# Kernel tuning notes

Hardware: AMD Instinct MI355X
Metric: run time of the kernel (lower is better)

The kernel has to match this reference:

```python
import jax, jax.numpy as jnp
import numpy as np

K, T, D, S, A, C, H = 128, 64, 128, 512, 4, 16, 512
N_LEAVES = 128
TEMP = 1.0          # sample_merge_temp
EPS_SQRT = 1e-4     # distances.EPSILON ** 0.5 with EPSILON = 1e-8
_SQ_EPS = 1e-12     # numerical guard inside sqrt (diagonal of pairwise dists is 0)


def setup_inputs() -> dict:
    key = jax.random.key(0)
    ks = jax.random.split(key, 11)
    leaf_counts_Kxt = jax.random.randint(ks[0], (K, T), 1, 5)
    embeddings_KxtxD = jax.random.normal(ks[1], (K, T, D), jnp.float32)
    log_felsensteins_KxtxSxA = jax.random.normal(ks[2], (K, T, S, A), jnp.float32)
    site_positions_SxC = jax.random.uniform(ks[3], (S, C), jnp.float32)
    W1 = jax.random.normal(ks[4], (2 * D, H), jnp.float32) / jnp.sqrt(2.0 * D)
    b1 = jnp.zeros((H,), jnp.float32)
    W2 = jax.random.normal(ks[5], (H, D), jnp.float32) / jnp.sqrt(1.0 * H)
    b2 = jnp.zeros((D,), jnp.float32)
    gumbel_Kxtt = jax.random.gumbel(ks[6], (K, T * T), jnp.float32)
    u1_K = jax.random.uniform(ks[7], (K,), jnp.float32, minval=1e-6, maxval=1.0)
    u2_K = jax.random.uniform(ks[8], (K,), jnp.float32, minval=1e-6, maxval=1.0)
    return {
        "N": N_LEAVES,
        "leaf_counts_Kxt": leaf_counts_Kxt,
        "embeddings_KxtxD": embeddings_KxtxD,
        "log_felsensteins_KxtxSxA": log_felsensteins_KxtxSxA,
        "site_positions_SxC": site_positions_SxC,
        "W1": W1, "b1": b1, "W2": W2, "b2": b2,
        "gumbel_Kxtt": gumbel_Kxtt, "u1_K": u1_K, "u2_K": u2_K,
    }


def _merge_encoder(c1_KxD, c2_KxD, W1, b1, W2, b2):
    # MLP merge encoder: MLP(concat(child1, child2)) -> parent embedding
    h = jax.nn.relu(jnp.concatenate([c1_KxD, c2_KxD], axis=-1) @ W1 + b1)
    return h @ W2 + b2


def reference(N, leaf_counts_Kxt, embeddings_KxtxD, log_felsensteins_KxtxSxA,
              site_positions_SxC, W1, b1, W2, b2, gumbel_Kxtt, u1_K, u2_K):
    Kp, t = leaf_counts_Kxt.shape
    ar = jnp.arange(Kp)

    # --- pairwise distances over all t*t subtree pairs per particle ---
    diff_Kxtxtxd = embeddings_KxtxD[:, :, None, :] - embeddings_KxtxD[:, None, :, :]
    pd_Kxtxt = jnp.sqrt(jnp.sum(diff_Kxtxtxd * diff_Kxtxtxd, axis=-1) + _SQ_EPS)
    merge_log_weights_Kxtxt = -pd_Kxtxt / TEMP
    # diagonal_scatter(-inf): forbid self-merges
    eye = jnp.eye(t, dtype=bool)[None]
    merge_log_weights_Kxtxt = jnp.where(eye, -jnp.inf, merge_log_weights_Kxtxt)

    # --- categorical merge sampling (gumbel-max with pre-drawn noise) ---
    flat_Kxtt = merge_log_weights_Kxtxt.reshape(Kp, t * t)
    sample_K = jnp.argmax(flat_Kxtt + gumbel_Kxtt, axis=1)
    idx1_K = sample_K // t
    idx2_K = sample_K % t
    log_merge_prob_K = (flat_Kxtt[ar, sample_K] + jnp.log(2.0)
                        - jax.scipy.special.logsumexp(flat_Kxtt, axis=1))

    # --- merged embedding ---
    child1_KxD = embeddings_KxtxD[ar, idx1_K]
    child2_KxD = embeddings_KxtxD[ar, idx2_K]
    embedding_KxD = _merge_encoder(child1_KxD, child2_KxD, W1, b1, W2, b2)

    # --- branch lengths sampled from Exp(rate = 1/(dist + eps)) ---
    d1_K = jnp.sqrt(jnp.sum((child1_KxD - embedding_KxD) ** 2, axis=-1) + _SQ_EPS)
    d2_K = jnp.sqrt(jnp.sum((child2_KxD - embedding_KxD) ** 2, axis=-1) + _SQ_EPS)
    rate1_K = 1.0 / (d1_K + EPS_SQRT)
    rate2_K = 1.0 / (d2_K + EPS_SQRT)
    branch1_K = -(1.0 / rate1_K) * jnp.log(u1_K)
    branch2_K = -(1.0 / rate2_K) * jnp.log(u2_K)
    log_branch1_prior_K = jnp.log(rate1_K) - rate1_K * branch1_K
    log_branch2_prior_K = jnp.log(rate2_K) - rate2_K * branch2_K

    log_v_plus_K = log_merge_prob_K + log_branch1_prior_K + log_branch2_prior_K

    # --- over-counting correction ---
    ones_K = jnp.sum(leaf_counts_Kxt == 1, axis=1)
    ones_K = ones_K - (leaf_counts_Kxt[ar, idx1_K] == 1).astype(ones_K.dtype)
    ones_K = ones_K - (leaf_counts_Kxt[ar, idx2_K] == 1).astype(ones_K.dtype)
    log_v_minus_K = jnp.log((N - ones_K).astype(jnp.float32))

    return (idx1_K, idx2_K, branch1_K, branch2_K, embedding_KxD,
            log_v_plus_K, log_v_minus_K)
```

## Files before the change

kernel.cpp:

```cpp
#include <hip/hip_runtime.h>
#include <math.h>

#define Kp 128
#define Tn 64
#define Dn 128
#define Hn 512
#define RS 136

typedef __attribute__((ext_vector_type(8))) short short8;
typedef __attribute__((ext_vector_type(4))) float f32x4;

__global__ __launch_bounds__(512, 1) void ep_kernel(
    const int*   __restrict__ Nptr,
    const int*   __restrict__ leaf,
    const float* __restrict__ emb,
    const float* __restrict__ W1,
    const float* __restrict__ b1,
    const float* __restrict__ W2,
    const float* __restrict__ b2,
    const float* __restrict__ gum,
    const float* __restrict__ u1,
    const float* __restrict__ u2,
    float* __restrict__ out)
{
    const int k    = blockIdx.x;
    const int tid  = threadIdx.x;
    const int lane = tid & 63;
    const int wid  = tid >> 6;

    __shared__ unsigned short EH[Tn * RS];
    __shared__ unsigned short EL[Tn * RS];
    __shared__ float xs[256];
    __shared__ float hsh[Hn];
    __shared__ float buf[2112];
    __shared__ float nI[Tn];
    __shared__ float sBest[8]; __shared__ int sIdx[8]; __shared__ float sW[8];
    __shared__ float sSum[8];
    __shared__ float sD1[2]; __shared__ float sD2[2];
    __shared__ int   sOnes;
    __shared__ int   fIdx; __shared__ float fW;
    __shared__ float embs[Dn];

    const bool gw   = (wid < 4);
    const int itp   = (wid >> 1) & 1;
    const int jtp   = wid & 1;
    const int lrow  = lane & 15;
    const int lq    = lane >> 4;

    if (tid < 64) {
        unsigned long long m = __ballot(leaf[k * Tn + tid] == 1);
        if (tid == 0) sOnes = __popcll(m);
    }

    float4 ev[4];
    {
        const float4* src = (const float4*)(emb + (size_t)k * Tn * Dn);
        #pragma unroll
        for (int it = 0; it < 4; ++it) ev[it] = src[tid + it * 512];
    }
    float gv[16];
    if (gw) {
        const float* gk = gum + (size_t)k * (Tn * Tn);
        #pragma unroll
        for (int a = 0; a < 2; ++a)
            #pragma unroll
            for (int b = 0; b < 2; ++b) {
                int it = 2 * itp + a, jt = 2 * jtp + b;
                int col = jt * 16 + lrow;
                #pragma unroll
                for (int r = 0; r < 4; ++r) {
                    int row = it * 16 + lq * 4 + r;
                    gv[(a * 2 + b) * 4 + r] = gk[row * Tn + col];
                }
            }
    }

    #pragma unroll
    for (int it = 0; it < 4; ++it) {
        int f4 = tid + it * 512;
        int i  = f4 >> 5;
        int d0 = (f4 & 31) << 2;
        float4 v = ev[it];
        unsigned short hx = __float_as_uint(v.x) >> 16, hy = __float_as_uint(v.y) >> 16,
                       hz = __float_as_uint(v.z) >> 16, hw = __float_as_uint(v.w) >> 16;
        float rx = v.x - __uint_as_float((unsigned int)hx << 16);
        float ry = v.y - __uint_as_float((unsigned int)hy << 16);
        float rz = v.z - __uint_as_float((unsigned int)hz << 16);
        float rw = v.w - __uint_as_float((unsigned int)hw << 16);
        unsigned short lx = __float_as_uint(rx) >> 16, ly = __float_as_uint(ry) >> 16,
                       lz = __float_as_uint(rz) >> 16, lw = __float_as_uint(rw) >> 16;
        *(ushort4*)&EH[i * RS + d0] = make_ushort4(hx, hy, hz, hw);
        *(ushort4*)&EL[i * RS + d0] = make_ushort4(lx, ly, lz, lw);
    }
    __syncthreads();

    f32x4 acc[2][2] = {};
    if (gw) {
        const int ka = lq * 8;
        #pragma unroll
        for (int ks = 0; ks < 4; ++ks) {
            int kb  = ks * 32 + ka;
            int ra0 = ((2 * itp + 0) * 16 + lrow) * RS + kb;
            int ra1 = ra0 + 16 * RS;
            int rb0 = ((2 * jtp + 0) * 16 + lrow) * RS + kb;
            int rb1 = rb0 + 16 * RS;
            short8 ah0 = *(const short8*)&EH[ra0], ah1 = *(const short8*)&EH[ra1];
            short8 al0 = *(const short8*)&EL[ra0], al1 = *(const short8*)&EL[ra1];
            short8 bh0 = *(const short8*)&EH[rb0], bh1 = *(const short8*)&EH[rb1];
            short8 bl0 = *(const short8*)&EL[rb0], bl1 = *(const short8*)&EL[rb1];
            acc[0][0] = __builtin_amdgcn_mfma_f32_16x16x32_bf16(ah0, bh0, acc[0][0], 0, 0, 0);
            acc[0][1] = __builtin_amdgcn_mfma_f32_16x16x32_bf16(ah0, bh1, acc[0][1], 0, 0, 0);
            acc[1][0] = __builtin_amdgcn_mfma_f32_16x16x32_bf16(ah1, bh0, acc[1][0], 0, 0, 0);
            acc[1][1] = __builtin_amdgcn_mfma_f32_16x16x32_bf16(ah1, bh1, acc[1][1], 0, 0, 0);
            acc[0][0] = __builtin_amdgcn_mfma_f32_16x16x32_bf16(ah0, bl0, acc[0][0], 0, 0, 0);
            acc[0][1] = __builtin_amdgcn_mfma_f32_16x16x32_bf16(ah0, bl1, acc[0][1], 0, 0, 0);
            acc[1][0] = __builtin_amdgcn_mfma_f32_16x16x32_bf16(ah1, bl0, acc[1][0], 0, 0, 0);
            acc[1][1] = __builtin_amdgcn_mfma_f32_16x16x32_bf16(ah1, bl1, acc[1][1], 0, 0, 0);
            acc[0][0] = __builtin_amdgcn_mfma_f32_16x16x32_bf16(al0, bh0, acc[0][0], 0, 0, 0);
            acc[0][1] = __builtin_amdgcn_mfma_f32_16x16x32_bf16(al0, bh1, acc[0][1], 0, 0, 0);
            acc[1][0] = __builtin_amdgcn_mfma_f32_16x16x32_bf16(al1, bh0, acc[1][0], 0, 0, 0);
            acc[1][1] = __builtin_amdgcn_mfma_f32_16x16x32_bf16(al1, bh1, acc[1][1], 0, 0, 0);
        }

        if (itp == jtp) {
            #pragma unroll
            for (int a = 0; a < 2; ++a) {
                if ((lrow >> 2) == lq) {
                    int c = lrow;
                    int t = 2 * itp + a;
                    f32x4 v = acc[a][a];
                    int   s = c & 3;
                    float val = (s == 0) ? v.x : (s == 1) ? v.y : (s == 2) ? v.z : v.w;
                    nI[t * 16 + c] = val;
                }
            }
        }
    }
    __syncthreads();

    float es = 0.0f, best = -INFINITY, bestW = 0.0f;
    int   bestIdx = 0;
    if (gw) {
        #pragma unroll
        for (int a = 0; a < 2; ++a)
            #pragma unroll
            for (int b = 0; b < 2; ++b) {
                int it = 2 * itp + a, jt = 2 * jtp + b;
                int col = jt * 16 + lrow;
                float njc = nI[col];
                f32x4 v = acc[a][b];
                float gvals[4] = {v.x, v.y, v.z, v.w};
                #pragma unroll
                for (int r = 0; r < 4; ++r) {
                    int row = it * 16 + lq * 4 + r;
                    float pd2 = nI[row] + njc - 2.0f * gvals[r];
                    pd2 = fmaxf(pd2, 0.0f) + 1e-12f;
                    float wv = (row == col) ? -INFINITY : -sqrtf(pd2);
                    es += expf(wv);
                    float wg = wv + gv[(a * 2 + b) * 4 + r];
                    int idx = row * Tn + col;
                    if (wg > best || (wg == best && idx < bestIdx)) {
                        best = wg; bestIdx = idx; bestW = wv;
                    }
                }
            }
    }

    #pragma unroll
    for (int off = 32; off > 0; off >>= 1) {
        float ob = __shfl_down(best, off);
        int   oi = __shfl_down(bestIdx, off);
        float ow = __shfl_down(bestW, off);
        float oe = __shfl_down(es, off);
        if (ob > best || (ob == best && oi < bestIdx)) { best = ob; bestIdx = oi; bestW = ow; }
        es += oe;
    }
    if (lane == 0) { sBest[wid] = best; sIdx[wid] = bestIdx; sW[wid] = bestW; sSum[wid] = es; }
    __syncthreads();
    if (tid == 0) {
        best = sBest[0]; bestIdx = sIdx[0]; bestW = sW[0];
        #pragma unroll
        for (int q = 1; q < 8; ++q) {
            if (sBest[q] > best || (sBest[q] == best && sIdx[q] < bestIdx)) {
                best = sBest[q]; bestIdx = sIdx[q]; bestW = sW[q];
            }
        }
        fIdx = bestIdx; fW = bestW;
    }
    __syncthreads();

    const int i1 = fIdx >> 6;
    const int i2 = fIdx & 63;

    if (tid < 256) {
        int d  = tid & 127;
        int ii = (tid < 128) ? i1 : i2;
        float hi = __uint_as_float((unsigned int)EH[ii * RS + d] << 16);
        float lo = __uint_as_float((unsigned int)EL[ii * RS + d] << 16);
        xs[tid] = hi + lo;
    }
    __syncthreads();

    {
        const int j0 = 4 * (tid & 127);
        const int ih = tid >> 7;
        const float* W1r = W1 + j0;
        float4 a = {0, 0, 0, 0};
        const int ib = ih * 64;
        #pragma unroll 4
        for (int i = ib; i < ib + 64; i += 4) {
            float4 x  = *(const float4*)&xs[i];
            float4 w0 = *(const float4*)&W1r[(size_t)(i + 0) * Hn];
            float4 w1 = *(const float4*)&W1r[(size_t)(i + 1) * Hn];
            float4 w2 = *(const float4*)&W1r[(size_t)(i + 2) * Hn];
            float4 w3 = *(const float4*)&W1r[(size_t)(i + 3) * Hn];
            a.x += x.x * w0.x + x.y * w1.x + x.z * w2.x + x.w * w3.x;
            a.y += x.x * w0.y + x.y * w1.y + x.z * w2.y + x.w * w3.y;
            a.z += x.x * w0.z + x.y * w1.z + x.z * w2.z + x.w * w3.z;
            a.w += x.x * w0.w + x.y * w1.w + x.z * w2.w + x.w * w3.w;
        }
        *(float4*)&buf[ih * 516 + j0] = a;
    }
    __syncthreads();
    hsh[tid] = fmaxf(b1[tid] + buf[tid] + buf[516 + tid]
                     + buf[1032 + tid] + buf[1548 + tid], 0.0f);
    __syncthreads();

    {
        const int jh  = tid >> 5;
        const int dd4 = 4 * (tid & 31);
        float4 a = {0, 0, 0, 0};
        const int jb = jh * 32;
        #pragma unroll 4
        for (int j = jb; j < jb + 32; j += 4) {
            float4 h4 = *(const float4*)&hsh[j];
            float4 w0 = *(const float4*)&W2[(size_t)(j + 0) * Dn + dd4];
            float4 w1 = *(const float4*)&W2[(size_t)(j + 1) * Dn + dd4];
            float4 w2 = *(const float4*)&W2[(size_t)(j + 2) * Dn + dd4];
            float4 w3 = *(const float4*)&W2[(size_t)(j + 3) * Dn + dd4];
            a.x += h4.x * w0.x + h4.y * w1.x + h4.z * w2.x + h4.w * w3.x;
            a.y += h4.x * w0.y + h4.y * w1.y + h4.z * w2.y + h4.w * w3.y;
            a.z += h4.x * w0.z + h4.y * w1.z + h4.z * w2.z + h4.w * w3.z;
            a.w += h4.x * w0.w + h4.y * w1.w + h4.z * w2.w + h4.w * w3.w;
        }
        *(float4*)&buf[jh * 132 + dd4] = a;
    }
    __syncthreads();
    if (tid < 128) {
        float e = b2[tid];
        #pragma unroll
        for (int p = 0; p < 16; ++p) e += buf[p * 132 + tid];
        embs[tid] = e;
        out[4 * Kp + k * Dn + tid] = e;
    }
    __syncthreads();

    if (tid < 128) {
        float e  = embs[tid];
        float q1 = xs[tid] - e;        float v1 = q1 * q1;
        float q2 = xs[128 + tid] - e;  float v2 = q2 * q2;
        #pragma unroll
        for (int off = 32; off > 0; off >>= 1) {
            v1 += __shfl_down(v1, off);
            v2 += __shfl_down(v2, off);
        }
        if (lane == 0) { sD1[wid] = v1; sD2[wid] = v2; }
    }
    __syncthreads();

    if (tid == 0) {
        float s1 = sD1[0] + sD1[1];
        float s2 = sD2[0] + sD2[1];
        float d1 = sqrtf(s1 + 1e-12f);
        float d2 = sqrtf(s2 + 1e-12f);
        float rate1 = 1.0f / (d1 + 1e-4f);
        float rate2 = 1.0f / (d2 + 1e-4f);
        float branch1 = -(1.0f / rate1) * logf(u1[k]);
        float branch2 = -(1.0f / rate2) * logf(u2[k]);
        float lbp1 = logf(rate1) - rate1 * branch1;
        float lbp2 = logf(rate2) - rate2 * branch2;
        float ssum = sSum[0] + sSum[1] + sSum[2] + sSum[3]
                   + sSum[4] + sSum[5] + sSum[6] + sSum[7];
        float lse  = logf(ssum);
        float lmp  = fW + 0.69314718055994531f - lse;
        float lvp  = lmp + lbp1 + lbp2;
        int lc1 = leaf[k * Tn + i1];
        int lc2 = leaf[k * Tn + i2];
        int ones = sOnes - (lc1 == 1 ? 1 : 0) - (lc2 == 1 ? 1 : 0);
        float lvm = logf((float)(Nptr[0] - ones));

        out[k]                         = (float)i1;
        out[Kp + k]                    = (float)i2;
        out[2 * Kp + k]                = branch1;
        out[3 * Kp + k]                = branch2;
        out[4 * Kp + Kp * Dn + k]      = lvp;
        out[4 * Kp + Kp * Dn + Kp + k] = lvm;
    }
}

extern "C" void kernel_launch(void* const* d_in, const int* in_sizes, int n_in,
                              void* d_out, int out_size, void* d_ws, size_t ws_size,
                              hipStream_t stream) {
    const int*   Nptr = (const int*)  d_in[0];
    const int*   leaf = (const int*)  d_in[1];
    const float* emb  = (const float*)d_in[2];
    const float* W1   = (const float*)d_in[5];
    const float* b1   = (const float*)d_in[6];
    const float* W2   = (const float*)d_in[7];
    const float* b2   = (const float*)d_in[8];
    const float* gum  = (const float*)d_in[9];
    const float* u1   = (const float*)d_in[10];
    const float* u2   = (const float*)d_in[11];
    float* out = (float*)d_out;

    ep_kernel<<<Kp, 512, 0, stream>>>(Nptr, leaf, emb, W1, b1, W2, b2, gum, u1, u2, out);
}
```

Before: 126.5 us.

## Prefetch MLP weights early, compute norms in fp32, and drop block barriers

Row squared norms are now computed in fp32 with shuffles during staging instead of being read from the MFMA diagonal, which removes one barrier. The first chunks of W1 and W2 are loaded into registers before the distance MFMA so their global latency overlaps that compute. The final argmax reduction is done redundantly by every thread, and child embeddings are rebuilt directly from the bf16 hi/lo shared arrays, which removes the xs/embs staging and several barriers. Small scalars (biases, u1/u2, N, leaf counts) are also loaded early. In exchange, register pressure goes up, and the fp32 norms may differ slightly from the MFMA-derived ones.

```diff
diff --git a/kernel.cpp b/kernel.cpp
--- a/kernel.cpp
+++ b/kernel.cpp
@@ -9,6 +9,10 @@
 
 typedef __attribute__((ext_vector_type(8))) short short8;
 typedef __attribute__((ext_vector_type(4))) float f32x4;
+
+__device__ __forceinline__ float bfpair(unsigned int hi_bits, unsigned int lo_bits) {
+    return __uint_as_float(hi_bits) + __uint_as_float(lo_bits);
+}
 
 __global__ __launch_bounds__(512, 1) void ep_kernel(
     const int*   __restrict__ Nptr,
@@ -30,16 +34,14 @@
 
     __shared__ unsigned short EH[Tn * RS];
     __shared__ unsigned short EL[Tn * RS];
-    __shared__ float xs[256];
     __shared__ float hsh[Hn];
     __shared__ float buf[2112];
     __shared__ float nI[Tn];
     __shared__ float sBest[8]; __shared__ int sIdx[8]; __shared__ float sW[8];
     __shared__ float sSum[8];
     __shared__ float sD1[2]; __shared__ float sD2[2];
+    __shared__ int   sLeaf[Tn];
     __shared__ int   sOnes;
-    __shared__ int   fIdx; __shared__ float fW;
-    __shared__ float embs[Dn];
 
     const bool gw   = (wid < 4);
     const int itp   = (wid >> 1) & 1;
@@ -47,8 +49,18 @@
     const int lrow  = lane & 15;
     const int lq    = lane >> 4;
 
+    const int j0  = 4 * (tid & 127);
+    const int ih  = tid >> 7;
+    const int ib  = ih * 64;
+    const float* W1r = W1 + j0;
+    const int jh  = tid >> 5;
+    const int jb  = jh * 32;
+    const int dd4 = 4 * (tid & 31);
+
     if (tid < 64) {
-        unsigned long long m = __ballot(leaf[k * Tn + tid] == 1);
+        int lc = leaf[k * Tn + tid];
+        sLeaf[tid] = lc;
+        unsigned long long m = __ballot(lc == 1);
         if (tid == 0) sOnes = __popcll(m);
     }
 
@@ -74,6 +86,10 @@
                 }
             }
     }
+    float b1v = b1[tid];
+    float b2v = (tid < 128) ? b2[tid] : 0.0f;
+    float u1v = 0.0f, u2v = 0.0f; int Nv = 0;
+    if (tid == 0) { u1v = u1[k]; u2v = u2[k]; Nv = Nptr[0]; }
 
     #pragma unroll
     for (int it = 0; it < 4; ++it) {
@@ -91,8 +107,23 @@
                        lz = __float_as_uint(rz) >> 16, lw = __float_as_uint(rw) >> 16;
         *(ushort4*)&EH[i * RS + d0] = make_ushort4(hx, hy, hz, hw);
         *(ushort4*)&EL[i * RS + d0] = make_ushort4(lx, ly, lz, lw);
-    }
-    __syncthreads();
+        float s = v.x * v.x + v.y * v.y + v.z * v.z + v.w * v.w;
+        s += __shfl_down(s, 16, 32);
+        s += __shfl_down(s,  8, 32);
+        s += __shfl_down(s,  4, 32);
+        s += __shfl_down(s,  2, 32);
+        s += __shfl_down(s,  1, 32);
+        if ((lane & 31) == 0) nI[i] = s;
+    }
+    __syncthreads();
+
+    float4 w1p[16];
+    #pragma unroll
+    for (int p = 0; p < 16; ++p) w1p[p] = *(const float4*)&W1r[(size_t)(ib + p) * Hn];
+    float4 w2p[8];
+    #pragma unroll
+    for (int p = 0; p < 8; ++p)  w2p[p] = *(const float4*)&W2[(size_t)(jb + p) * Dn + dd4];
+    __builtin_amdgcn_sched_barrier(0);
 
     f32x4 acc[2][2] = {};
     if (gw) {
@@ -121,22 +152,7 @@
             acc[1][0] = __builtin_amdgcn_mfma_f32_16x16x32_bf16(al1, bh0, acc[1][0], 0, 0, 0);
             acc[1][1] = __builtin_amdgcn_mfma_f32_16x16x32_bf16(al1, bh1, acc[1][1], 0, 0, 0);
         }
-
-        if (itp == jtp) {
-            #pragma unroll
-            for (int a = 0; a < 2; ++a) {
-                if ((lrow >> 2) == lq) {
-                    int c = lrow;
-                    int t = 2 * itp + a;
-                    f32x4 v = acc[a][a];
-                    int   s = c & 3;
-                    float val = (s == 0) ? v.x : (s == 1) ? v.y : (s == 2) ? v.z : v.w;
-                    nI[t * 16 + c] = val;
-                }
-            }
-        }
-    }
-    __syncthreads();
+    }
 
     float es = 0.0f, best = -INFINITY, bestW = 0.0f;
     int   bestIdx = 0;
@@ -165,7 +181,6 @@
                 }
             }
     }
-
     #pragma unroll
     for (int off = 32; off > 0; off >>= 1) {
         float ob = __shfl_down(best, off);
@@ -177,88 +192,100 @@
     }
     if (lane == 0) { sBest[wid] = best; sIdx[wid] = bestIdx; sW[wid] = bestW; sSum[wid] = es; }
     __syncthreads();
-    if (tid == 0) {
-        best = sBest[0]; bestIdx = sIdx[0]; bestW = sW[0];
-        #pragma unroll
-        for (int q = 1; q < 8; ++q) {
-            if (sBest[q] > best || (sBest[q] == best && sIdx[q] < bestIdx)) {
-                best = sBest[q]; bestIdx = sIdx[q]; bestW = sW[q];
-            }
-        }
-        fIdx = bestIdx; fW = bestW;
-    }
-    __syncthreads();
-
-    const int i1 = fIdx >> 6;
-    const int i2 = fIdx & 63;
-
-    if (tid < 256) {
-        int d  = tid & 127;
-        int ii = (tid < 128) ? i1 : i2;
-        float hi = __uint_as_float((unsigned int)EH[ii * RS + d] << 16);
-        float lo = __uint_as_float((unsigned int)EL[ii * RS + d] << 16);
-        xs[tid] = hi + lo;
-    }
-    __syncthreads();
+
+    float gBest = sBest[0], gW = sW[0], essum = sSum[0];
+    int   gIdx = sIdx[0];
+    #pragma unroll
+    for (int q = 1; q < 8; ++q) {
+        float bq = sBest[q]; int iq = sIdx[q];
+        if (bq > gBest || (bq == gBest && iq < gIdx)) { gBest = bq; gIdx = iq; gW = sW[q]; }
+        essum += sSum[q];
+    }
+    const int i1 = gIdx >> 6;
+    const int i2 = gIdx & 63;
 
     {
-        const int j0 = 4 * (tid & 127);
-        const int ih = tid >> 7;
-        const float* W1r = W1 + j0;
+        const int ii    = (ih < 2) ? i1 : i2;
+        const int dbase = (ih & 1) * 64;
+        const unsigned short* ehr = &EH[ii * RS + dbase];
+        const unsigned short* elr = &EL[ii * RS + dbase];
         float4 a = {0, 0, 0, 0};
-        const int ib = ih * 64;
+        #pragma unroll
+        for (int r = 0; r < 16; r += 4) {
+            uint2 hu = *(const uint2*)&ehr[r];
+            uint2 lu = *(const uint2*)&elr[r];
+            float x0 = bfpair(hu.x << 16,          lu.x << 16);
+            float x1 = bfpair(hu.x & 0xFFFF0000u,  lu.x & 0xFFFF0000u);
+            float x2 = bfpair(hu.y << 16,          lu.y << 16);
+            float x3 = bfpair(hu.y & 0xFFFF0000u,  lu.y & 0xFFFF0000u);
+            float4 w0 = w1p[r + 0], w1 = w1p[r + 1], w2 = w1p[r + 2], w3 = w1p[r + 3];
+            a.x += x0 * w0.x + x1 * w1.x + x2 * w2.x + x3 * w3.x;
+            a.y += x0 * w0.y + x1 * w1.y + x2 * w2.y + x3 * w3.y;
+            a.z += x0 * w0.z + x1 * w1.z + x2 * w2.z + x3 * w3.z;
+            a.w += x0 * w0.w + x1 * w1.w + x2 * w2.w + x3 * w3.w;
+        }
         #pragma unroll 4
-        for (int i = ib; i < ib + 64; i += 4) {
-            float4 x  = *(const float4*)&xs[i];
-            float4 w0 = *(const float4*)&W1r[(size_t)(i + 0) * Hn];
-            float4 w1 = *(const float4*)&W1r[(size_t)(i + 1) * Hn];
-            float4 w2 = *(const float4*)&W1r[(size_t)(i + 2) * Hn];
-            float4 w3 = *(const float4*)&W1r[(size_t)(i + 3) * Hn];
-            a.x += x.x * w0.x + x.y * w1.x + x.z * w2.x + x.w * w3.x;
-            a.y += x.x * w0.y + x.y * w1.y + x.z * w2.y + x.w * w3.y;
-            a.z += x.x * w0.z + x.y * w1.z + x.z * w2.z + x.w * w3.z;
-            a.w += x.x * w0.w + x.y * w1.w + x.z * w2.w + x.w * w3.w;
+        for (int r = 16; r < 64; r += 4) {
+            uint2 hu = *(const uint2*)&ehr[r];
+            uint2 lu = *(const uint2*)&elr[r];
+            float x0 = bfpair(hu.x << 16,          lu.x << 16);
+            float x1 = bfpair(hu.x & 0xFFFF0000u,  lu.x & 0xFFFF0000u);
+            float x2 = bfpair(hu.y << 16,          lu.y << 16);
+            float x3 = bfpair(hu.y & 0xFFFF0000u,  lu.y & 0xFFFF0000u);
+            float4 w0 = *(const float4*)&W1r[(size_t)(ib + r + 0) * Hn];
+            float4 w1 = *(const float4*)&W1r[(size_t)(ib + r + 1) * Hn];
+            float4 w2 = *(const float4*)&W1r[(size_t)(ib + r + 2) * Hn];
+            float4 w3 = *(const float4*)&W1r[(size_t)(ib + r + 3) * Hn];
+            a.x += x0 * w0.x + x1 * w1.x + x2 * w2.x + x3 * w3.x;
+            a.y += x0 * w0.y + x1 * w1.y + x2 * w2.y + x3 * w3.y;
+            a.z += x0 * w0.z + x1 * w1.z + x2 * w2.z + x3 * w3.z;
+            a.w += x0 * w0.w + x1 * w1.w + x2 * w2.w + x3 * w3.w;
         }
         *(float4*)&buf[ih * 516 + j0] = a;
     }
     __syncthreads();
-    hsh[tid] = fmaxf(b1[tid] + buf[tid] + buf[516 + tid]
+    hsh[tid] = fmaxf(b1v + buf[tid] + buf[516 + tid]
                      + buf[1032 + tid] + buf[1548 + tid], 0.0f);
     __syncthreads();
 
     {
-        const int jh  = tid >> 5;
-        const int dd4 = 4 * (tid & 31);
         float4 a = {0, 0, 0, 0};
-        const int jb = jh * 32;
-        #pragma unroll 4
-        for (int j = jb; j < jb + 32; j += 4) {
-            float4 h4 = *(const float4*)&hsh[j];
-            float4 w0 = *(const float4*)&W2[(size_t)(j + 0) * Dn + dd4];
-            float4 w1 = *(const float4*)&W2[(size_t)(j + 1) * Dn + dd4];
-            float4 w2 = *(const float4*)&W2[(size_t)(j + 2) * Dn + dd4];
-            float4 w3 = *(const float4*)&W2[(size_t)(j + 3) * Dn + dd4];
+        #pragma unroll
+        for (int j = 0; j < 8; j += 4) {
+            float4 h4 = *(const float4*)&hsh[jb + j];
+            float4 w0 = w2p[j + 0], w1 = w2p[j + 1], w2 = w2p[j + 2], w3 = w2p[j + 3];
             a.x += h4.x * w0.x + h4.y * w1.x + h4.z * w2.x + h4.w * w3.x;
             a.y += h4.x * w0.y + h4.y * w1.y + h4.z * w2.y + h4.w * w3.y;
             a.z += h4.x * w0.z + h4.y * w1.z + h4.z * w2.z + h4.w * w3.z;
             a.w += h4.x * w0.w + h4.y * w1.w + h4.z * w2.w + h4.w * w3.w;
         }
+        #pragma unroll 4
+        for (int j = 8; j < 32; j += 4) {
+            float4 h4 = *(const float4*)&hsh[jb + j];
+            float4 w0 = *(const float4*)&W2[(size_t)(jb + j + 0) * Dn + dd4];
+            float4 w1 = *(const float4*)&W2[(size_t)(jb + j + 1) * Dn + dd4];
+            float4 w2 = *(const float4*)&W2[(size_t)(jb + j + 2) * Dn + dd4];
+            float4 w3 = *(const float4*)&W2[(size_t)(jb + j + 3) * Dn + dd4];
+            a.x += h4.x * w0.x + h4.y * w1.x + h4.z * w2.x + h4.w * w3.x;
+            a.y += h4.x * w0.y + h4.y * w1.y + h4.z * w2.y + h4.w * w3.y;
+            a.z += h4.x * w0.z + h4.y * w1.z + h4.z * w2.z + h4.w * w3.z;
+            a.w += h4.x * w0.w + h4.y * w1.w + h4.z * w2.w + h4.w * w3.w;
+        }
         *(float4*)&buf[jh * 132 + dd4] = a;
     }
     __syncthreads();
+
     if (tid < 128) {
-        float e = b2[tid];
+        float e = b2v;
         #pragma unroll
         for (int p = 0; p < 16; ++p) e += buf[p * 132 + tid];
-        embs[tid] = e;
         out[4 * Kp + k * Dn + tid] = e;
-    }
-    __syncthreads();
-
-    if (tid < 128) {
-        float e  = embs[tid];
-        float q1 = xs[tid] - e;        float v1 = q1 * q1;
-        float q2 = xs[128 + tid] - e;  float v2 = q2 * q2;
+        float x1d = bfpair((unsigned int)EH[i1 * RS + tid] << 16,
+                           (unsigned int)EL[i1 * RS + tid] << 16);
+        float x2d = bfpair((unsigned int)EH[i2 * RS + tid] << 16,
+                           (unsigned int)EL[i2 * RS + tid] << 16);
+        float v1 = (x1d - e) * (x1d - e);
+        float v2 = (x2d - e) * (x2d - e);
         #pragma unroll
         for (int off = 32; off > 0; off >>= 1) {
             v1 += __shfl_down(v1, off);
@@ -275,19 +302,15 @@
         float d2 = sqrtf(s2 + 1e-12f);
         float rate1 = 1.0f / (d1 + 1e-4f);
         float rate2 = 1.0f / (d2 + 1e-4f);
-        float branch1 = -(1.0f / rate1) * logf(u1[k]);
-        float branch2 = -(1.0f / rate2) * logf(u2[k]);
+        float branch1 = -(1.0f / rate1) * logf(u1v);
+        float branch2 = -(1.0f / rate2) * logf(u2v);
         float lbp1 = logf(rate1) - rate1 * branch1;
         float lbp2 = logf(rate2) - rate2 * branch2;
-        float ssum = sSum[0] + sSum[1] + sSum[2] + sSum[3]
-                   + sSum[4] + sSum[5] + sSum[6] + sSum[7];
-        float lse  = logf(ssum);
-        float lmp  = fW + 0.69314718055994531f - lse;
+        float lse  = logf(essum);
+        float lmp  = gW + 0.69314718055994531f - lse;
         float lvp  = lmp + lbp1 + lbp2;
-        int lc1 = leaf[k * Tn + i1];
-        int lc2 = leaf[k * Tn + i2];
-        int ones = sOnes - (lc1 == 1 ? 1 : 0) - (lc2 == 1 ? 1 : 0);
-        float lvm = logf((float)(Nptr[0] - ones));
+        int ones = sOnes - (sLeaf[i1] == 1 ? 1 : 0) - (sLeaf[i2] == 1 ? 1 : 0);
+        float lvm = logf((float)(Nv - ones));
 
         out[k]                         = (float)i1;
         out[Kp + k]                    = (float)i2;
```

Result: no change. 127.5 us (+0.8%).
